# Optimization experiments

Hardware: AMD Instinct MI355X
Metric: run time of the kernel (lower is better)

The kernel has to match this reference:

```python
import jax, jax.numpy as jnp
import numpy as np

B, S, D, H = 2, 2048, 1024, 16
HD = D // H  # head_dim = 64


def setup_inputs() -> dict:
    key = jax.random.key(0)
    ks = jax.random.split(key, 9)
    s_in = 1.0 / np.sqrt(D)
    inp = {
        "hidden_state": jax.random.normal(ks[0], (B, S, D), dtype=jnp.float32),
        # per-head projections, stacked: [H, D, HD]
        "Wq": jax.random.uniform(ks[1], (H, D, HD), jnp.float32, -s_in, s_in),
        "bq": jax.random.uniform(ks[2], (H, HD), jnp.float32, -s_in, s_in),
        "Wk": jax.random.uniform(ks[3], (H, D, HD), jnp.float32, -s_in, s_in),
        "bk": jax.random.uniform(ks[4], (H, HD), jnp.float32, -s_in, s_in),
        "Wv": jax.random.uniform(ks[5], (H, D, HD), jnp.float32, -s_in, s_in),
        "bv": jax.random.uniform(ks[6], (H, HD), jnp.float32, -s_in, s_in),
        # output linear: [D, D]
        "Wo": jax.random.uniform(ks[7], (D, D), jnp.float32, -s_in, s_in),
        "bo": jax.random.uniform(ks[8], (D,), jnp.float32, -s_in, s_in),
    }
    return inp


def reference(hidden_state, Wq, bq, Wk, bk, Wv, bv, Wo, bo):
    # fused per-head projections: [B, H, S, HD]
    q = jnp.einsum("bsd,hde->bhse", hidden_state, Wq) + bq[None, :, None, :]
    k = jnp.einsum("bsd,hde->bhse", hidden_state, Wk) + bk[None, :, None, :]
    v = jnp.einsum("bsd,hde->bhse", hidden_state, Wv) + bv[None, :, None, :]
    scale = 1.0 / jnp.sqrt(jnp.float32(HD))
    scores = jnp.einsum("bhse,bhte->bhst", q, k) * scale  # [B, H, S, S]
    weights = jax.nn.softmax(scores, axis=-1)
    ctx = jnp.einsum("bhst,bhte->bhse", weights, v)       # [B, H, S, HD]
    # concat heads along last dim -> [B, S, D]
    ctx = jnp.transpose(ctx, (0, 2, 1, 3)).reshape(B, S, D)
    return ctx @ Wo + bo
```

## Files before the change

### kernel.cpp

```cpp
#include <hip/hip_runtime.h>
#include <hip/hip_bf16.h>
#include <math.h>

#define BB 2
#define SS 2048
#define DD 1024
#define HH 16
#define HD 64

typedef __attribute__((ext_vector_type(8))) _Float16 f16x8;
typedef __attribute__((ext_vector_type(2))) __fp16 fp16x2;
typedef __attribute__((ext_vector_type(8))) unsigned short u16x8;
typedef __attribute__((ext_vector_type(4))) float f32x4;
typedef __attribute__((ext_vector_type(4))) unsigned short u16x4;

__device__ __forceinline__ unsigned short hbits(_Float16 h) {
    union { _Float16 h; unsigned short s; } u; u.h = h; return u.s;
}

__device__ __forceinline__ int swz(int row, int grp) {
    return (row << 6) + (((grp) ^ (row & 7)) << 3);
}

__device__ __forceinline__ float fexp2(float x) {
#if __has_builtin(__builtin_amdgcn_exp2f)
    return __builtin_amdgcn_exp2f(x);
#else
    return exp2f(x);
#endif
}

__device__ __forceinline__ u16x4 pack4(float p0, float p1, float p2, float p3) {
#if __has_builtin(__builtin_amdgcn_cvt_pkrtz)
    union { fp16x2 h[2]; u16x4 u; } pu;
    pu.h[0] = __builtin_amdgcn_cvt_pkrtz(p0, p1);
    pu.h[1] = __builtin_amdgcn_cvt_pkrtz(p2, p3);
    return pu.u;
#else
    u16x4 r;
    r[0] = hbits((_Float16)p0); r[1] = hbits((_Float16)p1);
    r[2] = hbits((_Float16)p2); r[3] = hbits((_Float16)p3);
    return r;
#endif
}

__device__ __forceinline__ void gload_lds16(const unsigned short* g, unsigned short* l) {
#if __has_builtin(__builtin_amdgcn_global_load_lds)
    auto gp = (const __attribute__((address_space(1))) unsigned int*)(uintptr_t)g;
    auto lp = (__attribute__((address_space(3))) unsigned int*)(uintptr_t)l;
    __builtin_amdgcn_global_load_lds(gp, lp, 16, 0, 0);
#else
    *(u16x8*)(l + (threadIdx.x & 63) * 8) = *(const u16x8*)g;
#endif
}

__global__ __launch_bounds__(256) void prep_convert(
    const float* __restrict__ X,
    const float* __restrict__ Wq, const float* __restrict__ Wk,
    const float* __restrict__ Wv, const float* __restrict__ Wo,
    unsigned short* __restrict__ Xh, unsigned short* __restrict__ WT)
{
    __shared__ __align__(16) unsigned short LT[64 * 68];
    const int bid = blockIdx.x;
    const int tid = threadIdx.x;

    if (bid < 2048) {
        const int base = bid * 2048 + tid * 8;
        float4 a = *(const float4*)&X[base];
        float4 b = *(const float4*)&X[base + 4];
        u16x8 o;
        o[0] = hbits((_Float16)a.x); o[1] = hbits((_Float16)a.y);
        o[2] = hbits((_Float16)a.z); o[3] = hbits((_Float16)a.w);
        o[4] = hbits((_Float16)b.x); o[5] = hbits((_Float16)b.y);
        o[6] = hbits((_Float16)b.z); o[7] = hbits((_Float16)b.w);
        *(u16x8*)&Xh[base] = o;
        return;
    }

    const int t = bid - 2048;
    const float* src;
    size_t stride;
    int outRow0, kcol0;
    if (t < 768) {
        const int nt = t >> 4, ktile = t & 15;
        const int sel = nt >> 4, hh = nt & 15;
        const float* Ws = (sel == 0) ? Wq : ((sel == 1) ? Wk : Wv);
        src = Ws + (size_t)hh * (DD * HD) + (size_t)ktile * 64 * HD;
        stride = HD;
        outRow0 = nt * 64;
        kcol0 = ktile * 64;
    } else {
        const int tt = t - 768;
        const int nt = tt & 15, ktile = tt >> 4;
        src = Wo + (size_t)ktile * 64 * DD + nt * 64;
        stride = DD;
        outRow0 = 3072 + nt * 64;
        kcol0 = ktile * 64;
    }

    const int e = tid & 63, dq = tid >> 6;
#pragma unroll
    for (int p = 0; p < 16; p++) {
        const int dl = p * 4 + dq;
        LT[e * 68 + dl] = hbits((_Float16)src[(size_t)dl * stride + e]);
    }
    __syncthreads();
    const int eo = tid >> 2, d16 = (tid & 3) * 16;
#pragma unroll
    for (int j = 0; j < 4; j++) {
        *(ushort4*)&WT[(size_t)(outRow0 + eo) * DD + kcol0 + d16 + j * 4] =
            *(const ushort4*)&LT[eo * 68 + d16 + j * 4];
    }
}

#define GBM 128
#define GBN 128
#define GBK 64
#define NKT (DD / GBK)

__global__ __launch_bounds__(256) void qkv_gemm(
    const unsigned short* __restrict__ Xh, const unsigned short* __restrict__ WT,
    const float* __restrict__ bq, const float* __restrict__ bk,
    const float* __restrict__ bv,
    unsigned short* __restrict__ qh, unsigned short* __restrict__ kh,
    unsigned short* __restrict__ vTs, unsigned int* __restrict__ kc2)
{
    __shared__ __align__(16) unsigned short As[2][16 * 512];
    __shared__ __align__(16) unsigned short Bs[2][16 * 512];

    const int tid = threadIdx.x;
    const int m0 = blockIdx.y * GBM;
    const int n0 = blockIdx.x * GBN;
    const int lane = tid & 63;
    const int w = tid >> 6;
    const int wm = w & 1, wn = w >> 1;
    const int l15 = lane & 15, quad = lane >> 4;

    int g_off[4];
#pragma unroll
    for (int p = 0; p < 4; p++) {
        const int c = p * 4 + w;
        g_off[p] = ((c >> 1) * 16 + (lane & 15)) * DD + (c & 1) * 32 + (lane >> 4) * 8;
    }

    f32x4 acc[4][4];
#pragma unroll
    for (int i = 0; i < 4; i++)
#pragma unroll
        for (int j = 0; j < 4; j++) acc[i][j] = (f32x4){0.f, 0.f, 0.f, 0.f};

    const unsigned short* Abase = Xh + (size_t)m0 * DD;
    const unsigned short* Bbase = WT + (size_t)n0 * DD;

#pragma unroll
    for (int p = 0; p < 4; p++) {
        gload_lds16(Abase + g_off[p], &As[0][(p * 4 + w) * 512]);
        gload_lds16(Bbase + g_off[p], &Bs[0][(p * 4 + w) * 512]);
    }

    for (int it = 0; it < NKT; it++) {
        const int cur = it & 1;
        __syncthreads();
        if (it + 1 < NKT) {
            const int kt2 = (it + 1) * GBK;
#pragma unroll
            for (int p = 0; p < 4; p++) {
                gload_lds16(Abase + g_off[p] + kt2, &As[cur ^ 1][(p * 4 + w) * 512]);
                gload_lds16(Bbase + g_off[p] + kt2, &Bs[cur ^ 1][(p * 4 + w) * 512]);
            }
        }
#pragma unroll
        for (int ks = 0; ks < 2; ks++) {
            f16x8 af[4], bf[4];
#pragma unroll
            for (int i = 0; i < 4; i++) {
                af[i] = *(const f16x8*)&As[cur][((wm * 4 + i) * 2 + ks) * 512 + lane * 8];
                bf[i] = *(const f16x8*)&Bs[cur][((wn * 4 + i) * 2 + ks) * 512 + lane * 8];
            }
#pragma unroll
            for (int ns = 0; ns < 4; ns++)
#pragma unroll
                for (int ms = 0; ms < 4; ms++)
                    acc[ms][ns] = __builtin_amdgcn_mfma_f32_16x16x32_f16(
                        af[ms], bf[ns], acc[ms][ns], 0, 0, 0);
        }
    }

    const int sel = n0 >> 10;
    const int hw = ((n0 + wn * 64) >> 6) & 15;
    const int bblk = m0 >> 11;
    const float* bias = (sel == 0) ? bq : ((sel == 1) ? bk : bv);
    const size_t bh_base = ((size_t)bblk * HH + hw) * SS * HD;
    float wmx = 0.0f;
#pragma unroll
    for (int ms = 0; ms < 4; ms++) {
#pragma unroll
        for (int rr = 0; rr < 4; rr++) {
            const int m = m0 + wm * 64 + ms * 16 + quad * 4 + rr;
            const int s = m & (SS - 1);
            const int s63 = s & 63;
            float v2 = 0.0f;
#pragma unroll
            for (int ns = 0; ns < 4; ns++) {
                const int e = ns * 16 + l15;
                const float val = acc[ms][ns][rr] + bias[hw * HD + e];
                if (sel == 0) {
                    qh[bh_base + (size_t)s * HD + e] = hbits((_Float16)val);
                } else if (sel == 1) {
                    v2 = fmaf(val, val, v2);
                    const size_t kofs = bh_base + (size_t)(s >> 6) * 4096
                                      + swz(s63, e >> 3) + (e & 7);
                    kh[kofs] = hbits((_Float16)val);
                } else {
                    const size_t vofs = bh_base + (size_t)(s >> 6) * 4096
                                      + swz(e, s63 >> 3) + (s63 & 7);
                    vTs[vofs] = hbits((_Float16)val);
                }
            }
            if (sel == 1) {
                v2 += __shfl_xor(v2, 1);
                v2 += __shfl_xor(v2, 2);
                v2 += __shfl_xor(v2, 4);
                v2 += __shfl_xor(v2, 8);
                wmx = fmaxf(wmx, v2);
            }
        }
    }
    if (sel == 1) {
        wmx = fmaxf(wmx, __shfl_xor(wmx, 16));
        wmx = fmaxf(wmx, __shfl_xor(wmx, 32));
        if (lane == 0)
            atomicMax(&kc2[bblk * HH + hw], __float_as_uint(wmx));
    }
}

__global__ __launch_bounds__(256) void out_gemm(
    const unsigned short* __restrict__ Ctxh, const unsigned short* __restrict__ WoT,
    const float* __restrict__ bo, float* __restrict__ out)
{
    __shared__ __align__(16) unsigned short As[2][16 * 512];
    __shared__ __align__(16) unsigned short Bs[2][16 * 512];

    const int tid = threadIdx.x;
    const int m0 = blockIdx.y * GBM;
    const int n0 = blockIdx.x * GBN;
    const int lane = tid & 63;
    const int w = tid >> 6;
    const int wm = w & 1, wn = w >> 1;
    const int l15 = lane & 15, quad = lane >> 4;

    int g_off[4];
#pragma unroll
    for (int p = 0; p < 4; p++) {
        const int c = p * 4 + w;
        g_off[p] = ((c >> 1) * 16 + (lane & 15)) * DD + (c & 1) * 32 + (lane >> 4) * 8;
    }

    f32x4 acc[4][4];
#pragma unroll
    for (int i = 0; i < 4; i++)
#pragma unroll
        for (int j = 0; j < 4; j++) acc[i][j] = (f32x4){0.f, 0.f, 0.f, 0.f};

    const unsigned short* Abase = Ctxh + (size_t)m0 * DD;
    const unsigned short* Bbase = WoT + (size_t)n0 * DD;

#pragma unroll
    for (int p = 0; p < 4; p++) {
        gload_lds16(Abase + g_off[p], &As[0][(p * 4 + w) * 512]);
        gload_lds16(Bbase + g_off[p], &Bs[0][(p * 4 + w) * 512]);
    }

    for (int it = 0; it < NKT; it++) {
        const int cur = it & 1;
        __syncthreads();
        if (it + 1 < NKT) {
            const int kt2 = (it + 1) * GBK;
#pragma unroll
            for (int p = 0; p < 4; p++) {
                gload_lds16(Abase + g_off[p] + kt2, &As[cur ^ 1][(p * 4 + w) * 512]);
                gload_lds16(Bbase + g_off[p] + kt2, &Bs[cur ^ 1][(p * 4 + w) * 512]);
            }
        }
#pragma unroll
        for (int ks = 0; ks < 2; ks++) {
            f16x8 af[4], bf[4];
#pragma unroll
            for (int i = 0; i < 4; i++) {
                af[i] = *(const f16x8*)&As[cur][((wm * 4 + i) * 2 + ks) * 512 + lane * 8];
                bf[i] = *(const f16x8*)&Bs[cur][((wn * 4 + i) * 2 + ks) * 512 + lane * 8];
            }
#pragma unroll
            for (int ns = 0; ns < 4; ns++)
#pragma unroll
                for (int ms = 0; ms < 4; ms++)
                    acc[ms][ns] = __builtin_amdgcn_mfma_f32_16x16x32_f16(
                        af[ms], bf[ns], acc[ms][ns], 0, 0, 0);
        }
    }

#pragma unroll
    for (int ms = 0; ms < 4; ms++) {
#pragma unroll
        for (int rr = 0; rr < 4; rr++) {
            const size_t m = (size_t)(m0 + wm * 64 + ms * 16 + quad * 4 + rr);
#pragma unroll
            for (int ns = 0; ns < 4; ns++) {
                const int n = n0 + wn * 64 + ns * 16 + l15;
                out[m * DD + n] = acc[ms][ns][rr] + bo[n];
            }
        }
    }
}

#define TQB 128
#define TKB 64
#define NT (SS / TKB)
#define C1 0.1803368801111204f

__global__ __launch_bounds__(256) void attn_mfma(
    const unsigned short* __restrict__ qh, const unsigned short* __restrict__ kh,
    const unsigned short* __restrict__ vTs, const unsigned int* __restrict__ kc2,
    unsigned short* __restrict__ ctxh)
{
    __shared__ __align__(16) unsigned short KL [2][TKB * 64];
    __shared__ __align__(16) unsigned short VtL[2][HD * 64];
    __shared__ __align__(16) unsigned short PsL[4][32 * 64];

    const int tid  = threadIdx.x;
    const int lane = tid & 63;
    const int w    = tid >> 6;
    const int l15  = lane & 15;
    const int quad = lane >> 4;
    const int bh   = blockIdx.y;
    const int q0   = blockIdx.x * TQB;

    const float kfac = sqrtf(__uint_as_float(kc2[bh])) * 1.01f * C1;

    f16x8 qf[2][2];
    float M2[2];
#pragma unroll
    for (int msub = 0; msub < 2; msub++) {
        const unsigned short* qrow =
            qh + ((size_t)bh * SS + q0 + w * 32 + msub * 16 + l15) * HD;
        float nq2 = 0.0f;
#pragma unroll
        for (int dstep = 0; dstep < 2; dstep++) {
            qf[msub][dstep] = *(const f16x8*)&qrow[dstep * 32 + quad * 8];
#pragma unroll
            for (int j = 0; j < 8; j++) {
                const float x = (float)qf[msub][dstep][j];
                nq2 = fmaf(x, x, nq2);
            }
        }
        nq2 += __shfl_xor(nq2, 16);
        nq2 += __shfl_xor(nq2, 32);
        M2[msub] = sqrtf(nq2) * kfac;
    }

    f16x8 ones;
#pragma unroll
    for (int j = 0; j < 8; j++) ones[j] = (_Float16)1.0f;

    f32x4 o[2][4], lones[2];
#pragma unroll
    for (int ms = 0; ms < 2; ms++) {
        lones[ms] = (f32x4){0.f, 0.f, 0.f, 0.f};
#pragma unroll
        for (int e = 0; e < 4; e++) o[ms][e] = (f32x4){0.f, 0.f, 0.f, 0.f};
    }

    const unsigned short* kb0 = kh  + (size_t)bh * SS * HD;
    const unsigned short* vb0 = vTs + (size_t)bh * SS * HD;

    gload_lds16(kb0 + tid * 8,        &KL [0][w * 512]);
    gload_lds16(kb0 + 2048 + tid * 8, &KL [0][2048 + w * 512]);
    gload_lds16(vb0 + tid * 8,        &VtL[0][w * 512]);
    gload_lds16(vb0 + 2048 + tid * 8, &VtL[0][2048 + w * 512]);

    for (int t = 0; t < NT; t++) {
        const int cur = t & 1;
        __syncthreads();
        if (t + 1 < NT) {
            const unsigned short* kb = kb0 + (size_t)(t + 1) * 4096;
            const unsigned short* vb = vb0 + (size_t)(t + 1) * 4096;
            gload_lds16(kb + tid * 8,        &KL [cur ^ 1][w * 512]);
            gload_lds16(kb + 2048 + tid * 8, &KL [cur ^ 1][2048 + w * 512]);
            gload_lds16(vb + tid * 8,        &VtL[cur ^ 1][w * 512]);
            gload_lds16(vb + 2048 + tid * 8, &VtL[cur ^ 1][2048 + w * 512]);
        }

        f32x4 sc[2][4];
#pragma unroll
        for (int ksub = 0; ksub < 4; ksub++) {
            const int row = ksub * 16 + l15;
            f16x8 k0 = *(const f16x8*)&KL[cur][swz(row, quad)];
            f16x8 k1 = *(const f16x8*)&KL[cur][swz(row, 4 + quad)];
#pragma unroll
            for (int msub = 0; msub < 2; msub++) {
                f32x4 a = (f32x4){0.f, 0.f, 0.f, 0.f};
                a = __builtin_amdgcn_mfma_f32_16x16x32_f16(k0, qf[msub][0], a, 0, 0, 0);
                a = __builtin_amdgcn_mfma_f32_16x16x32_f16(k1, qf[msub][1], a, 0, 0, 0);
                sc[msub][ksub] = a;
            }
        }

#pragma unroll
        for (int msub = 0; msub < 2; msub++) {
            const int prow = msub * 16 + l15;
#pragma unroll
            for (int ksub = 0; ksub < 4; ksub++) {
                const float p0 = fexp2(fmaf(sc[msub][ksub][0], C1, -M2[msub]));
                const float p1 = fexp2(fmaf(sc[msub][ksub][1], C1, -M2[msub]));
                const float p2 = fexp2(fmaf(sc[msub][ksub][2], C1, -M2[msub]));
                const float p3 = fexp2(fmaf(sc[msub][ksub][3], C1, -M2[msub]));
                *(u16x4*)&PsL[w][swz(prow, ksub * 2 + (quad >> 1)) + (quad & 1) * 4] =
                    pack4(p0, p1, p2, p3);
            }
        }

#pragma unroll
        for (int kj = 0; kj < 2; kj++) {
            f16x8 pa[2];
#pragma unroll
            for (int msub = 0; msub < 2; msub++)
                pa[msub] = *(const f16x8*)&PsL[w][swz(msub * 16 + l15, kj * 4 + quad)];
            lones[0] = __builtin_amdgcn_mfma_f32_16x16x32_f16(pa[0], ones, lones[0], 0, 0, 0);
            lones[1] = __builtin_amdgcn_mfma_f32_16x16x32_f16(pa[1], ones, lones[1], 0, 0, 0);
#pragma unroll
            for (int esub = 0; esub < 4; esub++) {
                f16x8 vr = *(const f16x8*)&VtL[cur][swz(esub * 16 + l15, kj * 4 + quad)];
                o[0][esub] = __builtin_amdgcn_mfma_f32_16x16x32_f16(pa[0], vr, o[0][esub], 0, 0, 0);
                o[1][esub] = __builtin_amdgcn_mfma_f32_16x16x32_f16(pa[1], vr, o[1][esub], 0, 0, 0);
            }
        }
    }

    const int b = bh >> 4;
    const int h = bh & 15;
#pragma unroll
    for (int msub = 0; msub < 2; msub++) {
#pragma unroll
        for (int rr = 0; rr < 4; rr++) {
            const float linv = 1.0f / lones[msub][rr];
            const int row = q0 + w * 32 + msub * 16 + quad * 4 + rr;
#pragma unroll
            for (int esub = 0; esub < 4; esub++) {
                ctxh[((size_t)b * SS + row) * DD + h * HD + esub * 16 + l15] =
                    hbits((_Float16)(o[msub][esub][rr] * linv));
            }
        }
    }
}

extern "C" void kernel_launch(void* const* d_in, const int* in_sizes, int n_in,
                              void* d_out, int out_size, void* d_ws, size_t ws_size,
                              hipStream_t stream) {
    const float* X  = (const float*)d_in[0];
    const float* Wq = (const float*)d_in[1];
    const float* bq = (const float*)d_in[2];
    const float* Wk = (const float*)d_in[3];
    const float* bk = (const float*)d_in[4];
    const float* Wv = (const float*)d_in[5];
    const float* bv = (const float*)d_in[6];
    const float* Wo = (const float*)d_in[7];
    const float* bo = (const float*)d_in[8];
    float* out = (float*)d_out;

    const size_t NB2 = (size_t)4096 * 1024 * 2;
    unsigned char* w8 = (unsigned char*)d_ws;
    unsigned short* Xh   = (unsigned short*)(w8);
    unsigned short* WT   = (unsigned short*)(w8 + NB2);
    unsigned short* qh   = (unsigned short*)(w8 + 2 * NB2);
    unsigned short* kh   = (unsigned short*)(w8 + 3 * NB2);
    unsigned short* vTs  = (unsigned short*)(w8 + 4 * NB2);
    unsigned short* ctxh = (unsigned short*)(w8 + 5 * NB2);
    unsigned int*   kc2  = (unsigned int*)(w8 + 6 * NB2);
    unsigned short* WoT  = WT + (size_t)3072 * 1024;

    (void)hipMemsetAsync(kc2, 0, BB * HH * sizeof(unsigned int), stream);

    prep_convert<<<dim3(3072), 256, 0, stream>>>(X, Wq, Wk, Wv, Wo, Xh, WT);

    qkv_gemm<<<dim3(3072 / GBN, 4096 / GBM), 256, 0, stream>>>(
        Xh, WT, bq, bk, bv, qh, kh, vTs, kc2);

    attn_mfma<<<dim3(SS / TQB, BB * HH), 256, 0, stream>>>(qh, kh, vTs, kc2, ctxh);

    out_gemm<<<dim3(1024 / GBN, 4096 / GBM), 256, 0, stream>>>(ctxh, WoT, bo, out);
}
```

Before: 235.6 us.

## Restructure QKV GEMM into 256x256 tiles with 8-wave ping-pong pipeline

Rewrites the QKV projection GEMM to use 256x256 output tiles computed by 512-thread blocks of 8 waves. The K loop is split into four MFMA phases that interleave global-to-LDS staging of the next A/B halves, using explicit s_barrier, vmcnt waits and s_setprio. It also remaps block IDs so neighbouring tiles land on the same XCD. The aim is more data reuse per tile and better overlap of memory traffic with MFMA work, at the cost of more registers and LDS per block and a fragile hand-tuned wait/barrier schedule.

```diff
diff --git a/kernel.cpp b/kernel.cpp
--- a/kernel.cpp
+++ b/kernel.cpp
@@ -118,92 +118,164 @@
 #define GBK 64
 #define NKT (DD / GBK)
 
-__global__ __launch_bounds__(256) void qkv_gemm(
+__global__ __launch_bounds__(512, 2) void qkv_gemm(
     const unsigned short* __restrict__ Xh, const unsigned short* __restrict__ WT,
     const float* __restrict__ bq, const float* __restrict__ bk,
     const float* __restrict__ bv,
     unsigned short* __restrict__ qh, unsigned short* __restrict__ kh,
     unsigned short* __restrict__ vTs, unsigned int* __restrict__ kc2)
 {
-    __shared__ __align__(16) unsigned short As[2][16 * 512];
-    __shared__ __align__(16) unsigned short Bs[2][16 * 512];
-
-    const int tid = threadIdx.x;
-    const int m0 = blockIdx.y * GBM;
-    const int n0 = blockIdx.x * GBN;
+    __shared__ __align__(16) unsigned short As[2][2][8192];
+    __shared__ __align__(16) unsigned short Bs[2][2][8192];
+
+    const int tid  = threadIdx.x;
     const int lane = tid & 63;
-    const int w = tid >> 6;
-    const int wm = w & 1, wn = w >> 1;
-    const int l15 = lane & 15, quad = lane >> 4;
-
-    int g_off[4];
-#pragma unroll
-    for (int p = 0; p < 4; p++) {
-        const int c = p * 4 + w;
-        g_off[p] = ((c >> 1) * 16 + (lane & 15)) * DD + (c & 1) * 32 + (lane >> 4) * 8;
-    }
-
-    f32x4 acc[4][4];
-#pragma unroll
-    for (int i = 0; i < 4; i++)
-#pragma unroll
-        for (int j = 0; j < 4; j++) acc[i][j] = (f32x4){0.f, 0.f, 0.f, 0.f};
+    const int w    = tid >> 6;
+    const int wm   = w >> 2;
+    const int wn   = w & 3;
+    const int l15  = lane & 15, quad = lane >> 4;
+
+    const int bid = blockIdx.x;
+    const int sid = (bid & 7) * 24 + (bid >> 3);
+    const int tn = sid % 12, tm = sid / 12;
+    const int m0 = tm * 256, n0 = tn * 256;
+
+    const int off0 = ((w >> 1) * 16 + l15) * DD + (w & 1) * 32 + quad * 8;
 
     const unsigned short* Abase = Xh + (size_t)m0 * DD;
     const unsigned short* Bbase = WT + (size_t)n0 * DD;
 
-#pragma unroll
-    for (int p = 0; p < 4; p++) {
-        gload_lds16(Abase + g_off[p], &As[0][(p * 4 + w) * 512]);
-        gload_lds16(Bbase + g_off[p], &Bs[0][(p * 4 + w) * 512]);
-    }
-
-    for (int it = 0; it < NKT; it++) {
-        const int cur = it & 1;
-        __syncthreads();
-        if (it + 1 < NKT) {
-            const int kt2 = (it + 1) * GBK;
-#pragma unroll
-            for (int p = 0; p < 4; p++) {
-                gload_lds16(Abase + g_off[p] + kt2, &As[cur ^ 1][(p * 4 + w) * 512]);
-                gload_lds16(Bbase + g_off[p] + kt2, &Bs[cur ^ 1][(p * 4 + w) * 512]);
-            }
-        }
-#pragma unroll
-        for (int ks = 0; ks < 2; ks++) {
-            f16x8 af[4], bf[4];
-#pragma unroll
-            for (int i = 0; i < 4; i++) {
-                af[i] = *(const f16x8*)&As[cur][((wm * 4 + i) * 2 + ks) * 512 + lane * 8];
-                bf[i] = *(const f16x8*)&Bs[cur][((wn * 4 + i) * 2 + ks) * 512 + lane * 8];
-            }
-#pragma unroll
-            for (int ns = 0; ns < 4; ns++)
-#pragma unroll
-                for (int ms = 0; ms < 4; ms++)
-                    acc[ms][ns] = __builtin_amdgcn_mfma_f32_16x16x32_f16(
-                        af[ms], bf[ns], acc[ms][ns], 0, 0, 0);
-        }
+    auto STAGE = [&](unsigned short* ls, const unsigned short* gb) {
+        gload_lds16(gb + off0,            ls + w * 512);
+        gload_lds16(gb + off0 + 64 * DD,  ls + (w + 8) * 512);
+    };
+
+    f32x4 acc[8][4];
+#pragma unroll
+    for (int i = 0; i < 8; i++)
+#pragma unroll
+        for (int j = 0; j < 4; j++) acc[i][j] = (f32x4){0.f, 0.f, 0.f, 0.f};
+
+    STAGE(&As[0][0][0], Abase);
+    STAGE(&As[0][1][0], Abase + 128 * DD);
+    STAGE(&Bs[0][0][0], Bbase);
+    STAGE(&Bs[0][1][0], Bbase + 128 * DD);
+    STAGE(&As[1][0][0], Abase + 64);
+    STAGE(&As[1][1][0], Abase + 128 * DD + 64);
+    asm volatile("s_waitcnt vmcnt(4)" ::: "memory");
+    __builtin_amdgcn_s_barrier();
+
+    const int bch = (wn & 1) * 8;
+
+    for (int T = 0; T < NKT; ++T) {
+        const int buf = T & 1;
+        const unsigned short* Ar = &As[buf][wm][0];
+        const unsigned short* Br = &Bs[buf][wn >> 1][0];
+        f16x8 af[8][2], bf[4][2];
+
+        if (T + 1 < NKT) STAGE(&Bs[(T + 1) & 1][0][0], Bbase + (size_t)(T + 1) * 64);
+#pragma unroll
+        for (int mf = 0; mf < 4; ++mf)
+#pragma unroll
+            for (int ks = 0; ks < 2; ++ks)
+                af[mf][ks] = *(const f16x8*)&Ar[(mf * 2 + ks) * 512 + lane * 8];
+#pragma unroll
+        for (int nf = 0; nf < 2; ++nf)
+#pragma unroll
+            for (int ks = 0; ks < 2; ++ks)
+                bf[nf][ks] = *(const f16x8*)&Br[(bch + nf * 2 + ks) * 512 + lane * 8];
+        __builtin_amdgcn_s_barrier();
+        asm volatile("s_waitcnt lgkmcnt(0)" ::: "memory");
+        __builtin_amdgcn_sched_barrier(0);
+        __builtin_amdgcn_s_setprio(1);
+#pragma unroll
+        for (int ks = 0; ks < 2; ++ks)
+#pragma unroll
+            for (int mf = 0; mf < 4; ++mf)
+#pragma unroll
+                for (int nf = 0; nf < 2; ++nf)
+                    acc[mf][nf] = __builtin_amdgcn_mfma_f32_16x16x32_f16(
+                        af[mf][ks], bf[nf][ks], acc[mf][nf], 0, 0, 0);
+        __builtin_amdgcn_s_setprio(0);
+        __builtin_amdgcn_s_barrier();
+
+        if (T + 1 < NKT) STAGE(&Bs[(T + 1) & 1][1][0], Bbase + 128 * DD + (size_t)(T + 1) * 64);
+#pragma unroll
+        for (int mf = 4; mf < 8; ++mf)
+#pragma unroll
+            for (int ks = 0; ks < 2; ++ks)
+                af[mf][ks] = *(const f16x8*)&Ar[(mf * 2 + ks) * 512 + lane * 8];
+#pragma unroll
+        for (int nf = 2; nf < 4; ++nf)
+#pragma unroll
+            for (int ks = 0; ks < 2; ++ks)
+                bf[nf][ks] = *(const f16x8*)&Br[(bch + nf * 2 + ks) * 512 + lane * 8];
+        __builtin_amdgcn_s_barrier();
+        asm volatile("s_waitcnt lgkmcnt(0)" ::: "memory");
+        __builtin_amdgcn_sched_barrier(0);
+        __builtin_amdgcn_s_setprio(1);
+#pragma unroll
+        for (int ks = 0; ks < 2; ++ks)
+#pragma unroll
+            for (int mf = 4; mf < 8; ++mf)
+#pragma unroll
+                for (int nf = 2; nf < 4; ++nf)
+                    acc[mf][nf] = __builtin_amdgcn_mfma_f32_16x16x32_f16(
+                        af[mf][ks], bf[nf][ks], acc[mf][nf], 0, 0, 0);
+        __builtin_amdgcn_s_setprio(0);
+        __builtin_amdgcn_s_barrier();
+
+        if (T + 2 < NKT) STAGE(&As[buf][0][0], Abase + (size_t)(T + 2) * 64);
+        __builtin_amdgcn_s_barrier();
+        __builtin_amdgcn_s_setprio(1);
+#pragma unroll
+        for (int ks = 0; ks < 2; ++ks)
+#pragma unroll
+            for (int mf = 0; mf < 4; ++mf)
+#pragma unroll
+                for (int nf = 2; nf < 4; ++nf)
+                    acc[mf][nf] = __builtin_amdgcn_mfma_f32_16x16x32_f16(
+                        af[mf][ks], bf[nf][ks], acc[mf][nf], 0, 0, 0);
+        __builtin_amdgcn_s_setprio(0);
+        __builtin_amdgcn_s_barrier();
+
+        if (T + 2 < NKT) STAGE(&As[buf][1][0], Abase + 128 * DD + (size_t)(T + 2) * 64);
+        if (T < NKT - 2) {
+            asm volatile("s_waitcnt vmcnt(4)" ::: "memory");
+        } else if (T == NKT - 2) {
+            asm volatile("s_waitcnt vmcnt(0)" ::: "memory");
+        }
+        __builtin_amdgcn_s_barrier();
+        __builtin_amdgcn_s_setprio(1);
+#pragma unroll
+        for (int ks = 0; ks < 2; ++ks)
+#pragma unroll
+            for (int mf = 4; mf < 8; ++mf)
+#pragma unroll
+                for (int nf = 0; nf < 2; ++nf)
+                    acc[mf][nf] = __builtin_amdgcn_mfma_f32_16x16x32_f16(
+                        af[mf][ks], bf[nf][ks], acc[mf][nf], 0, 0, 0);
+        __builtin_amdgcn_s_setprio(0);
+        __builtin_amdgcn_s_barrier();
     }
 
     const int sel = n0 >> 10;
     const int hw = ((n0 + wn * 64) >> 6) & 15;
-    const int bblk = m0 >> 11;
     const float* bias = (sel == 0) ? bq : ((sel == 1) ? bk : bv);
-    const size_t bh_base = ((size_t)bblk * HH + hw) * SS * HD;
     float wmx = 0.0f;
 #pragma unroll
-    for (int ms = 0; ms < 4; ms++) {
-#pragma unroll
-        for (int rr = 0; rr < 4; rr++) {
-            const int m = m0 + wm * 64 + ms * 16 + quad * 4 + rr;
+    for (int mf = 0; mf < 8; ++mf) {
+#pragma unroll
+        for (int rr = 0; rr < 4; ++rr) {
+            const int m = m0 + wm * 128 + mf * 16 + quad * 4 + rr;
             const int s = m & (SS - 1);
             const int s63 = s & 63;
+            const size_t bh_base = ((size_t)(m >> 11) * HH + hw) * SS * HD;
             float v2 = 0.0f;
 #pragma unroll
-            for (int ns = 0; ns < 4; ns++) {
-                const int e = ns * 16 + l15;
-                const float val = acc[ms][ns][rr] + bias[hw * HD + e];
+            for (int nf = 0; nf < 4; ++nf) {
+                const int e = nf * 16 + l15;
+                const float val = acc[mf][nf][rr] + bias[hw * HD + e];
                 if (sel == 0) {
                     qh[bh_base + (size_t)s * HD + e] = hbits((_Float16)val);
                 } else if (sel == 1) {
@@ -230,7 +302,7 @@
         wmx = fmaxf(wmx, __shfl_xor(wmx, 16));
         wmx = fmaxf(wmx, __shfl_xor(wmx, 32));
         if (lane == 0)
-            atomicMax(&kc2[bblk * HH + hw], __float_as_uint(wmx));
+            atomicMax(&kc2[(m0 >> 11) * HH + hw], __float_as_uint(wmx));
     }
 }
 
@@ -482,7 +554,7 @@
 
     prep_convert<<<dim3(3072), 256, 0, stream>>>(X, Wq, Wk, Wv, Wo, Xh, WT);
 
-    qkv_gemm<<<dim3(3072 / GBN, 4096 / GBM), 256, 0, stream>>>(
+    qkv_gemm<<<dim3(192), 512, 0, stream>>>(
         Xh, WT, bq, bk, bv, qh, kh, vTs, kc2);
 
     attn_mfma<<<dim3(SS / TQB, BB * HH), 256, 0, stream>>>(qh, kh, vTs, kc2, ctxh);
```

Measured after the change: 222.0 us. 1.06x faster.
